# Kernel tuning notes

Measured on AMD Instinct MI355X. Metric: run time of the kernel, lower is better.

The kernel has to match this reference:

```python
import jax, jax.numpy as jnp
import numpy as np

K = 4            # n_factors
AGG_PARAM = 0.5
EPS = 1e-12      # F.normalize eps


def _normalize(v):
    # F.normalize along last axis: v / max(||v||, eps)
    return v / jnp.maximum(jnp.linalg.norm(v, axis=-1, keepdims=True), EPS)


def _aggregate(x, nbrs, max_iter):
    # x: [b, n, d], nbrs: [n, m] with values in [0, n] (n -> zero pad row)
    b, n, d = x.shape
    m = nbrs.shape[-1]
    dd = d // K
    xk = _normalize(x.reshape(b, n, K, dd))            # [b,n,k,dd]
    z_src = jnp.concatenate(
        [xk.reshape(b, n, d), jnp.zeros((b, 1, d), x.dtype)], axis=1)
    z = z_src[:, nbrs.reshape(-1)].reshape(b, n, m, K, dd)  # gather neighbors
    u = None
    for it in range(max_iter):
        if u is None:
            p = jnp.full((b, n, m, K), 1.0 / K, x.dtype)  # softmax of zeros
        else:
            logits = jnp.einsum('bnmkd,bnkd->bnmk', z, u)
            p = jax.nn.softmax(logits, axis=3)
        u = jnp.einsum('bnmkd,bnmk->bnkd', z, p) + xk
        if it < max_iter - 1:
            u = _normalize(u)
    return u.reshape(b, n, d)


def setup_inputs() -> dict:
    key = jax.random.key(0)
    k1, k2 = jax.random.split(key)
    T, b, n, d, m = 3, 1, 50000, 64, 16
    x_all = jax.random.normal(k1, (T, b, n, d), dtype=jnp.float32)
    neighbors_all = jax.random.randint(k2, (T, n, m), 0, n, dtype=jnp.int64)
    return {"x_all": x_all, "neighbors_all": neighbors_all, "max_iter": 3}


def reference(x_all, neighbors_all, max_iter):
    T = x_all.shape[0]
    embs = []
    for t in range(T):
        x_temp = _aggregate(x_all[t], neighbors_all[t], max_iter)
        if t > 0:
            w = jax.nn.sigmoid(
                jnp.arange(t, dtype=x_all.dtype)).reshape(t, 1, 1, 1)
            e = (jnp.sum(w * jnp.stack(embs), axis=0) / t * AGG_PARAM
                 + x_temp * (1.0 - AGG_PARAM))
        else:
            e = x_temp
        embs.append(e)
    return jnp.stack(embs)  # [T, b, n, d]
```

## Files before the change

### kernel.cpp

```cpp
#include <hip/hip_runtime.h>


constexpr int T  = 3;
constexpr int N  = 50000;
constexpr int D  = 64;
constexpr int M  = 16;
constexpr float EPS2 = 1e-24f;

template <int CTRL>
__device__ __forceinline__ float dpp_add(float v) {
    int rot = __builtin_amdgcn_mov_dpp(__float_as_int(v), CTRL, 0xF, 0xF, false);
    return v + __int_as_float(rot);
}
__device__ __forceinline__ float rowsum16(float v) {
    v = dpp_add<0x128>(v);
    v = dpp_add<0x124>(v);
    v = dpp_add<0x122>(v);
    v = dpp_add<0x121>(v);
    return v;
}

__global__ __launch_bounds__(256, 4) void eaconv_fused(
    const float* __restrict__ x_all,
    const int*   __restrict__ nbr_all,
    float*       __restrict__ out)
{
    __shared__ float zb[4][M * D];
    __shared__ float ub[4][D];
    __shared__ float wb[4][D];
    const int wv   = threadIdx.x >> 6;
    const int i    = blockIdx.x * 4 + wv;
    const int lane = threadIdx.x & 63;
    if (i >= N) return;
    const int p  = lane & 15;
    const int k  = lane >> 4;
    const int x7 = p & 7;
    float* zw = zb[wv];
    float* uw = ub[wv];
    float* wwp = wb[wv];

    const int gq = lane >> 2;
    const int ge = lane & 3;
    const int c4 = (4 * k) ^ x7;

    float acc = 0.f;
    const float s1q = 0.25f * 0.7310585786300049f;

#pragma unroll
    for (int t = 0; t < T; ++t) {
        const float* x = x_all + (size_t)t * N * D;
        int j = nbr_all[((size_t)t * N + i) * M + p];
        const bool valid = (unsigned)j < (unsigned)N;
        j = valid ? j : 0;

#pragma unroll
        for (int c = 0; c < 4; ++c) {
            const int mm = 4 * c + k;
            const int jr = __shfl(j, mm, 64);
            const float4 v = *(const float4*)(x + (size_t)jr * D + p * 4);
            *(float4*)&zw[mm * 64 + ((p ^ (mm & 7)) << 2)] = v;
        }

        const float xv = x[(size_t)i * D + lane];
        const float sx = rowsum16(xv * xv);
        const float xh = xv * __builtin_amdgcn_rsqf(fmaxf(sx, EPS2));

        float zrow[16];
#pragma unroll
        for (int q = 0; q < 4; ++q) {
            const float4 v = *(const float4*)&zw[p * 64 + ((c4 ^ q) << 2)];
            zrow[4*q+0] = v.x; zrow[4*q+1] = v.y;
            zrow[4*q+2] = v.z; zrow[4*q+3] = v.w;
        }
        float zr[16];
#pragma unroll
        for (int m = 0; m < 16; ++m)
            zr[m] = zw[m * 64 + ((gq ^ (m & 7)) << 2) + ge];

        float s0 = zrow[0]*zrow[0], s1 = zrow[1]*zrow[1],
              s2 = zrow[2]*zrow[2], s3 = zrow[3]*zrow[3];
#pragma unroll
        for (int q = 4; q < 16; q += 4) {
            s0 = fmaf(zrow[q+0], zrow[q+0], s0);
            s1 = fmaf(zrow[q+1], zrow[q+1], s1);
            s2 = fmaf(zrow[q+2], zrow[q+2], s2);
            s3 = fmaf(zrow[q+3], zrow[q+3], s3);
        }
        float rz = __builtin_amdgcn_rsqf(fmaxf((s0+s1)+(s2+s3), EPS2));
        if (!valid) rz = 0.f;

        wwp[k * 16 + p] = rz;
        float rzr[16];
#pragma unroll
        for (int q = 0; q < 4; ++q) {
            const float4 v = *(const float4*)&wwp[k * 16 + 4 * q];
            rzr[4*q+0] = v.x; rzr[4*q+1] = v.y;
            rzr[4*q+2] = v.z; rzr[4*q+3] = v.w;
        }
        float u = xh * 4.0f;
#pragma unroll
        for (int m = 0; m < 16; ++m) u = fmaf(rzr[m], zr[m], u);
        float inv = __builtin_amdgcn_rsqf(fmaxf(rowsum16(u * u), EPS2));
        uw[lane] = u;

#pragma unroll
        for (int it = 1; it < 3; ++it) {
            float urow[16];
#pragma unroll
            for (int q = 0; q < 4; ++q) {
                const float4 v = *(const float4*)&uw[k * 16 + 4 * q];
                urow[4*q+0] = v.x; urow[4*q+1] = v.y;
                urow[4*q+2] = v.z; urow[4*q+3] = v.w;
            }
            float d0 = zrow[0]*urow[0], d1 = zrow[1]*urow[1],
                  d2 = zrow[2]*urow[2], d3 = zrow[3]*urow[3];
#pragma unroll
            for (int q = 4; q < 16; q += 4) {
                d0 = fmaf(zrow[q+0], urow[q+0], d0);
                d1 = fmaf(zrow[q+1], urow[q+1], d1);
                d2 = fmaf(zrow[q+2], urow[q+2], d2);
                d3 = fmaf(zrow[q+3], urow[q+3], d3);
            }
            const float dot = (d0 + d1) + (d2 + d3);
            const float logit = dot * (rz * inv);
            const float e = __expf(logit);
            float es = e + __shfl_xor(e, 16, 64);
            es += __shfl_xor(es, 32, 64);
            const float wf = e * __builtin_amdgcn_rcpf(es) * rz;

            wwp[k * 16 + p] = wf;
            float wr[16];
#pragma unroll
            for (int q = 0; q < 4; ++q) {
                const float4 v = *(const float4*)&wwp[k * 16 + 4 * q];
                wr[4*q+0] = v.x; wr[4*q+1] = v.y;
                wr[4*q+2] = v.z; wr[4*q+3] = v.w;
            }
            u = xh;
#pragma unroll
            for (int m = 0; m < 16; ++m) u = fmaf(wr[m], zr[m], u);
            if (it < 2) {
                inv = __builtin_amdgcn_rsqf(fmaxf(rowsum16(u * u), EPS2));
                uw[lane] = u;
            }
        }

        float wout;
        if (t == 0)      { wout = u; acc = u; }
        else if (t == 1) { wout = 0.25f * acc + 0.5f * u;
                           acc = fmaf(s1q, wout, 0.125f * acc); }
        else             { wout = acc + 0.5f * u; }
        out[((size_t)t * N + i) * D + lane] = wout;
    }
}

extern "C" void kernel_launch(void* const* d_in, const int* in_sizes, int n_in,
                              void* d_out, int out_size, void* d_ws, size_t ws_size,
                              hipStream_t stream) {
    const float* x_all = (const float*)d_in[0];
    const int*   nbrs  = (const int*)d_in[1];
    float*       out   = (float*)d_out;

    const int blocks = (N + 3) / 4;
    eaconv_fused<<<blocks, 256, 0, stream>>>(x_all, nbrs, out);
}
```

Before: 183.4 us.

## Prefetch next timestep's neighbor gather and split LDS into two layouts

Loads the next timestep's neighbor indices, self row and neighbor rows into registers while the current timestep computes, so global gather latency overlaps with compute. Gathered rows are now written to two LDS buffers: a swizzled one for row reads and a padded (stride 65) one for column reads. This replaces the XOR-swizzled column access and is meant to cut bank conflicts and address math. It costs more LDS per block and more live registers (four float4 prefetch buffers), which may reduce occupancy.

```diff
diff --git a/kernel.cpp b/kernel.cpp
--- a/kernel.cpp
+++ b/kernel.cpp
@@ -25,7 +25,8 @@
     const int*   __restrict__ nbr_all,
     float*       __restrict__ out)
 {
-    __shared__ float zb[4][M * D];
+    __shared__ float zs[4][M * 64];
+    __shared__ float zp[4][M * 65];
     __shared__ float ub[4][D];
     __shared__ float wb[4][D];
     const int wv   = threadIdx.x >> 6;
@@ -35,47 +36,76 @@
     const int p  = lane & 15;
     const int k  = lane >> 4;
     const int x7 = p & 7;
-    float* zw = zb[wv];
-    float* uw = ub[wv];
+    char* zsb = (char*)zs[wv];
+    char* zpb = (char*)zp[wv];
+    float* uw  = ub[wv];
     float* wwp = wb[wv];
 
-    const int gq = lane >> 2;
-    const int ge = lane & 3;
-    const int c4 = (4 * k) ^ x7;
+    const int ve  = 256 * k + 16 * (p ^ k);
+    const int vo  = ve ^ 64;
+    const int vpw = 260 * k + 16 * p;
+    const int c4  = (4 * k) ^ x7;
+    const int rq0 = 256 * p + ((c4 ^ 0) << 4);
+    const int rq1 = 256 * p + ((c4 ^ 1) << 4);
+    const int rq2 = 256 * p + ((c4 ^ 2) << 4);
+    const int rq3 = 256 * p + ((c4 ^ 3) << 4);
+    const int colb = 4 * lane;
+    const int rowb = 64 * k;
 
     float acc = 0.f;
     const float s1q = 0.25f * 0.7310585786300049f;
 
+    int jc; bool valid; float xv; float4 g0, g1, g2, g3;
+    {
+        const int jr = nbr_all[(size_t)i * M + p];
+        valid = (unsigned)jr < (unsigned)N;
+        jc = valid ? jr : 0;
+        xv = x_all[(size_t)i * D + lane];
+        const int j0 = __shfl(jc,      k, 64), j1 = __shfl(jc,  4 + k, 64),
+                  j2 = __shfl(jc,  8 + k, 64), j3 = __shfl(jc, 12 + k, 64);
+        g0 = *(const float4*)(x_all + (size_t)j0 * D + 4 * p);
+        g1 = *(const float4*)(x_all + (size_t)j1 * D + 4 * p);
+        g2 = *(const float4*)(x_all + (size_t)j2 * D + 4 * p);
+        g3 = *(const float4*)(x_all + (size_t)j3 * D + 4 * p);
+    }
+
 #pragma unroll
     for (int t = 0; t < T; ++t) {
-        const float* x = x_all + (size_t)t * N * D;
-        int j = nbr_all[((size_t)t * N + i) * M + p];
-        const bool valid = (unsigned)j < (unsigned)N;
-        j = valid ? j : 0;
-
-#pragma unroll
-        for (int c = 0; c < 4; ++c) {
-            const int mm = 4 * c + k;
-            const int jr = __shfl(j, mm, 64);
-            const float4 v = *(const float4*)(x + (size_t)jr * D + p * 4);
-            *(float4*)&zw[mm * 64 + ((p ^ (mm & 7)) << 2)] = v;
-        }
-
-        const float xv = x[(size_t)i * D + lane];
+        *(float4*)(zsb + ve)         = g0;
+        *(float4*)(zsb + vo + 1024)  = g1;
+        *(float4*)(zsb + ve + 2048)  = g2;
+        *(float4*)(zsb + vo + 3072)  = g3;
+        *(float4*)(zpb + vpw)        = g0;
+        *(float4*)(zpb + vpw + 1040) = g1;
+        *(float4*)(zpb + vpw + 2080) = g2;
+        *(float4*)(zpb + vpw + 3120) = g3;
+
+        int jn = 0; bool nvalid = false; float xn = 0.f;
+        if (t < T - 1) {
+            const int jr = nbr_all[((size_t)(t + 1) * N + i) * M + p];
+            nvalid = (unsigned)jr < (unsigned)N;
+            jn = nvalid ? jr : 0;
+            xn = x_all[((size_t)(t + 1) * N + i) * D + lane];
+        }
+
         const float sx = rowsum16(xv * xv);
         const float xh = xv * __builtin_amdgcn_rsqf(fmaxf(sx, EPS2));
 
         float zrow[16];
-#pragma unroll
-        for (int q = 0; q < 4; ++q) {
-            const float4 v = *(const float4*)&zw[p * 64 + ((c4 ^ q) << 2)];
-            zrow[4*q+0] = v.x; zrow[4*q+1] = v.y;
-            zrow[4*q+2] = v.z; zrow[4*q+3] = v.w;
+        {
+            const float4 v0 = *(const float4*)(zsb + rq0);
+            const float4 v1 = *(const float4*)(zsb + rq1);
+            const float4 v2 = *(const float4*)(zsb + rq2);
+            const float4 v3 = *(const float4*)(zsb + rq3);
+            zrow[ 0]=v0.x; zrow[ 1]=v0.y; zrow[ 2]=v0.z; zrow[ 3]=v0.w;
+            zrow[ 4]=v1.x; zrow[ 5]=v1.y; zrow[ 6]=v1.z; zrow[ 7]=v1.w;
+            zrow[ 8]=v2.x; zrow[ 9]=v2.y; zrow[10]=v2.z; zrow[11]=v2.w;
+            zrow[12]=v3.x; zrow[13]=v3.y; zrow[14]=v3.z; zrow[15]=v3.w;
         }
         float zr[16];
 #pragma unroll
         for (int m = 0; m < 16; ++m)
-            zr[m] = zw[m * 64 + ((gq ^ (m & 7)) << 2) + ge];
+            zr[m] = *(const float*)(zpb + colb + 260 * m);
 
         float s0 = zrow[0]*zrow[0], s1 = zrow[1]*zrow[1],
               s2 = zrow[2]*zrow[2], s3 = zrow[3]*zrow[3];
@@ -89,13 +119,17 @@
         float rz = __builtin_amdgcn_rsqf(fmaxf((s0+s1)+(s2+s3), EPS2));
         if (!valid) rz = 0.f;
 
-        wwp[k * 16 + p] = rz;
+        wwp[lane] = rz;
         float rzr[16];
-#pragma unroll
-        for (int q = 0; q < 4; ++q) {
-            const float4 v = *(const float4*)&wwp[k * 16 + 4 * q];
-            rzr[4*q+0] = v.x; rzr[4*q+1] = v.y;
-            rzr[4*q+2] = v.z; rzr[4*q+3] = v.w;
+        {
+            const float4 v0 = *(const float4*)((char*)wwp + rowb);
+            const float4 v1 = *(const float4*)((char*)wwp + rowb + 16);
+            const float4 v2 = *(const float4*)((char*)wwp + rowb + 32);
+            const float4 v3 = *(const float4*)((char*)wwp + rowb + 48);
+            rzr[ 0]=v0.x; rzr[ 1]=v0.y; rzr[ 2]=v0.z; rzr[ 3]=v0.w;
+            rzr[ 4]=v1.x; rzr[ 5]=v1.y; rzr[ 6]=v1.z; rzr[ 7]=v1.w;
+            rzr[ 8]=v2.x; rzr[ 9]=v2.y; rzr[10]=v2.z; rzr[11]=v2.w;
+            rzr[12]=v3.x; rzr[13]=v3.y; rzr[14]=v3.z; rzr[15]=v3.w;
         }
         float u = xh * 4.0f;
 #pragma unroll
@@ -103,14 +137,28 @@
         float inv = __builtin_amdgcn_rsqf(fmaxf(rowsum16(u * u), EPS2));
         uw[lane] = u;
 
+        if (t < T - 1) {
+            const float* xnp = x_all + (size_t)(t + 1) * N * D;
+            const int j0 = __shfl(jn,      k, 64), j1 = __shfl(jn,  4 + k, 64),
+                      j2 = __shfl(jn,  8 + k, 64), j3 = __shfl(jn, 12 + k, 64);
+            g0 = *(const float4*)(xnp + (size_t)j0 * D + 4 * p);
+            g1 = *(const float4*)(xnp + (size_t)j1 * D + 4 * p);
+            g2 = *(const float4*)(xnp + (size_t)j2 * D + 4 * p);
+            g3 = *(const float4*)(xnp + (size_t)j3 * D + 4 * p);
+        }
+
 #pragma unroll
         for (int it = 1; it < 3; ++it) {
             float urow[16];
-#pragma unroll
-            for (int q = 0; q < 4; ++q) {
-                const float4 v = *(const float4*)&uw[k * 16 + 4 * q];
-                urow[4*q+0] = v.x; urow[4*q+1] = v.y;
-                urow[4*q+2] = v.z; urow[4*q+3] = v.w;
+            {
+                const float4 v0 = *(const float4*)((char*)uw + rowb);
+                const float4 v1 = *(const float4*)((char*)uw + rowb + 16);
+                const float4 v2 = *(const float4*)((char*)uw + rowb + 32);
+                const float4 v3 = *(const float4*)((char*)uw + rowb + 48);
+                urow[ 0]=v0.x; urow[ 1]=v0.y; urow[ 2]=v0.z; urow[ 3]=v0.w;
+                urow[ 4]=v1.x; urow[ 5]=v1.y; urow[ 6]=v1.z; urow[ 7]=v1.w;
+                urow[ 8]=v2.x; urow[ 9]=v2.y; urow[10]=v2.z; urow[11]=v2.w;
+                urow[12]=v3.x; urow[13]=v3.y; urow[14]=v3.z; urow[15]=v3.w;
             }
             float d0 = zrow[0]*urow[0], d1 = zrow[1]*urow[1],
                   d2 = zrow[2]*urow[2], d3 = zrow[3]*urow[3];
@@ -128,13 +176,17 @@
             es += __shfl_xor(es, 32, 64);
             const float wf = e * __builtin_amdgcn_rcpf(es) * rz;
 
-            wwp[k * 16 + p] = wf;
+            wwp[lane] = wf;
             float wr[16];
-#pragma unroll
-            for (int q = 0; q < 4; ++q) {
-                const float4 v = *(const float4*)&wwp[k * 16 + 4 * q];
-                wr[4*q+0] = v.x; wr[4*q+1] = v.y;
-                wr[4*q+2] = v.z; wr[4*q+3] = v.w;
+            {
+                const float4 v0 = *(const float4*)((char*)wwp + rowb);
+                const float4 v1 = *(const float4*)((char*)wwp + rowb + 16);
+                const float4 v2 = *(const float4*)((char*)wwp + rowb + 32);
+                const float4 v3 = *(const float4*)((char*)wwp + rowb + 48);
+                wr[ 0]=v0.x; wr[ 1]=v0.y; wr[ 2]=v0.z; wr[ 3]=v0.w;
+                wr[ 4]=v1.x; wr[ 5]=v1.y; wr[ 6]=v1.z; wr[ 7]=v1.w;
+                wr[ 8]=v2.x; wr[ 9]=v2.y; wr[10]=v2.z; wr[11]=v2.w;
+                wr[12]=v3.x; wr[13]=v3.y; wr[14]=v3.z; wr[15]=v3.w;
             }
             u = xh;
 #pragma unroll
@@ -151,6 +203,8 @@
                            acc = fmaf(s1q, wout, 0.125f * acc); }
         else             { wout = acc + 0.5f * u; }
         out[((size_t)t * N + i) * D + lane] = wout;
+
+        jc = jn; valid = nvalid; xv = xn;
     }
 }
 
```

Result: slower. 200.4 us (+9.3%).

## Keep per-neighbor factor rows in registers and reduce via DPP instead of LDS

Applied to the files above, without the earlier changes.

Each lane now loads its own neighbor row's four float4 chunks directly, reading them in a strided order. It also keeps a full 16-element factor row of x, z and u in registers. Cross-neighbor sums use rowsum16 DPP reductions instead of LDS round-trips for the rz, softmax weight and u arrays, which removes two shared buffers and several LDS writes and reads per iteration. The cost is more DPP reduction ops per element (16 rowsums per iteration), higher register pressure, and output stores from only 4 lanes per row. The bounds check is dropped, which relies on N being divisible by 4.

```diff
diff --git a/kernel.cpp b/kernel.cpp
--- a/kernel.cpp
+++ b/kernel.cpp
@@ -1,10 +1,10 @@
 #include <hip/hip_runtime.h>
 
 
-constexpr int T  = 3;
-constexpr int N  = 50000;
-constexpr int D  = 64;
-constexpr int M  = 16;
+constexpr int T = 3;
+constexpr int N = 50000;
+constexpr int D = 64;
+constexpr int M = 16;
 constexpr float EPS2 = 1e-24f;
 
 template <int CTRL>
@@ -25,25 +25,26 @@
     const int*   __restrict__ nbr_all,
     float*       __restrict__ out)
 {
-    __shared__ float zb[4][M * D];
-    __shared__ float ub[4][D];
-    __shared__ float wb[4][D];
+    __shared__ float zs[4][M * 64];
     const int wv   = threadIdx.x >> 6;
     const int i    = blockIdx.x * 4 + wv;
     const int lane = threadIdx.x & 63;
-    if (i >= N) return;
     const int p  = lane & 15;
     const int k  = lane >> 4;
     const int x7 = p & 7;
-    float* zw = zb[wv];
-    float* uw = ub[wv];
-    float* wwp = wb[wv];
+    char* zsb = (char*)zs[wv];
 
-    const int gq = lane >> 2;
-    const int ge = lane & 3;
-    const int c4 = (4 * k) ^ x7;
+    const int wa0 = 256 * p + (((k     ) ^ x7) << 4);
+    const int wa1 = 256 * p + (((k |  4) ^ x7) << 4);
+    const int wa2 = 256 * p + (((k |  8) ^ x7) << 4);
+    const int wa3 = 256 * p + (((k | 12) ^ x7) << 4);
+    const int c4  = (4 * k) ^ x7;
+    const int ra0 = 256 * p + ((c4 ^ 0) << 4);
+    const int ra1 = 256 * p + ((c4 ^ 1) << 4);
+    const int ra2 = 256 * p + ((c4 ^ 2) << 4);
+    const int ra3 = 256 * p + ((c4 ^ 3) << 4);
 
-    float acc = 0.f;
+    float accr[16];
     const float s1q = 0.25f * 0.7310585786300049f;
 
 #pragma unroll
@@ -53,104 +54,122 @@
         const bool valid = (unsigned)j < (unsigned)N;
         j = valid ? j : 0;
 
-#pragma unroll
-        for (int c = 0; c < 4; ++c) {
-            const int mm = 4 * c + k;
-            const int jr = __shfl(j, mm, 64);
-            const float4 v = *(const float4*)(x + (size_t)jr * D + p * 4);
-            *(float4*)&zw[mm * 64 + ((p ^ (mm & 7)) << 2)] = v;
-        }
+        const float* zbase = x + (size_t)j * D + 4 * k;
+        const float4 g0 = *(const float4*)(zbase +  0);
+        const float4 g1 = *(const float4*)(zbase + 16);
+        const float4 g2 = *(const float4*)(zbase + 32);
+        const float4 g3 = *(const float4*)(zbase + 48);
 
-        const float xv = x[(size_t)i * D + lane];
-        const float sx = rowsum16(xv * xv);
-        const float xh = xv * __builtin_amdgcn_rsqf(fmaxf(sx, EPS2));
+        const float4* xr4 = (const float4*)(x + (size_t)i * D + 16 * k);
+        const float4 h0 = xr4[0], h1 = xr4[1], h2 = xr4[2], h3 = xr4[3];
 
-        float zrow[16];
-#pragma unroll
-        for (int q = 0; q < 4; ++q) {
-            const float4 v = *(const float4*)&zw[p * 64 + ((c4 ^ q) << 2)];
-            zrow[4*q+0] = v.x; zrow[4*q+1] = v.y;
-            zrow[4*q+2] = v.z; zrow[4*q+3] = v.w;
-        }
-        float zr[16];
-#pragma unroll
-        for (int m = 0; m < 16; ++m)
-            zr[m] = zw[m * 64 + ((gq ^ (m & 7)) << 2) + ge];
+        *(float4*)(zsb + wa0) = g0;
+        *(float4*)(zsb + wa1) = g1;
+        *(float4*)(zsb + wa2) = g2;
+        *(float4*)(zsb + wa3) = g3;
 
-        float s0 = zrow[0]*zrow[0], s1 = zrow[1]*zrow[1],
-              s2 = zrow[2]*zrow[2], s3 = zrow[3]*zrow[3];
+        float xh[16] = {h0.x,h0.y,h0.z,h0.w, h1.x,h1.y,h1.z,h1.w,
+                        h2.x,h2.y,h2.z,h2.w, h3.x,h3.y,h3.z,h3.w};
+        float a0 = xh[0]*xh[0], a1 = xh[1]*xh[1],
+              a2 = xh[2]*xh[2], a3 = xh[3]*xh[3];
 #pragma unroll
         for (int q = 4; q < 16; q += 4) {
-            s0 = fmaf(zrow[q+0], zrow[q+0], s0);
-            s1 = fmaf(zrow[q+1], zrow[q+1], s1);
-            s2 = fmaf(zrow[q+2], zrow[q+2], s2);
-            s3 = fmaf(zrow[q+3], zrow[q+3], s3);
+            a0 = fmaf(xh[q+0], xh[q+0], a0);
+            a1 = fmaf(xh[q+1], xh[q+1], a1);
+            a2 = fmaf(xh[q+2], xh[q+2], a2);
+            a3 = fmaf(xh[q+3], xh[q+3], a3);
         }
-        float rz = __builtin_amdgcn_rsqf(fmaxf((s0+s1)+(s2+s3), EPS2));
+        const float rx = __builtin_amdgcn_rsqf(fmaxf((a0+a1)+(a2+a3), EPS2));
+#pragma unroll
+        for (int q = 0; q < 16; ++q) xh[q] *= rx;
+
+        const float4 z0 = *(const float4*)(zsb + ra0);
+        const float4 z1 = *(const float4*)(zsb + ra1);
+        const float4 z2 = *(const float4*)(zsb + ra2);
+        const float4 z3 = *(const float4*)(zsb + ra3);
+        float zh[16] = {z0.x,z0.y,z0.z,z0.w, z1.x,z1.y,z1.z,z1.w,
+                        z2.x,z2.y,z2.z,z2.w, z3.x,z3.y,z3.z,z3.w};
+        float b0 = zh[0]*zh[0], b1 = zh[1]*zh[1],
+              b2 = zh[2]*zh[2], b3 = zh[3]*zh[3];
+#pragma unroll
+        for (int q = 4; q < 16; q += 4) {
+            b0 = fmaf(zh[q+0], zh[q+0], b0);
+            b1 = fmaf(zh[q+1], zh[q+1], b1);
+            b2 = fmaf(zh[q+2], zh[q+2], b2);
+            b3 = fmaf(zh[q+3], zh[q+3], b3);
+        }
+        float rz = __builtin_amdgcn_rsqf(fmaxf((b0+b1)+(b2+b3), EPS2));
         if (!valid) rz = 0.f;
+#pragma unroll
+        for (int q = 0; q < 16; ++q) zh[q] *= rz;
 
-        wwp[k * 16 + p] = rz;
-        float rzr[16];
+        float ur[16];
 #pragma unroll
-        for (int q = 0; q < 4; ++q) {
-            const float4 v = *(const float4*)&wwp[k * 16 + 4 * q];
-            rzr[4*q+0] = v.x; rzr[4*q+1] = v.y;
-            rzr[4*q+2] = v.z; rzr[4*q+3] = v.w;
+        for (int q = 0; q < 16; ++q)
+            ur[q] = fmaf(xh[q], 4.0f, rowsum16(zh[q]));
+        float n0 = ur[0]*ur[0], n1 = ur[1]*ur[1],
+              n2 = ur[2]*ur[2], n3 = ur[3]*ur[3];
+#pragma unroll
+        for (int q = 4; q < 16; q += 4) {
+            n0 = fmaf(ur[q+0], ur[q+0], n0);
+            n1 = fmaf(ur[q+1], ur[q+1], n1);
+            n2 = fmaf(ur[q+2], ur[q+2], n2);
+            n3 = fmaf(ur[q+3], ur[q+3], n3);
         }
-        float u = xh * 4.0f;
-#pragma unroll
-        for (int m = 0; m < 16; ++m) u = fmaf(rzr[m], zr[m], u);
-        float inv = __builtin_amdgcn_rsqf(fmaxf(rowsum16(u * u), EPS2));
-        uw[lane] = u;
+        float inv = __builtin_amdgcn_rsqf(fmaxf((n0+n1)+(n2+n3), EPS2));
 
 #pragma unroll
         for (int it = 1; it < 3; ++it) {
-            float urow[16];
-#pragma unroll
-            for (int q = 0; q < 4; ++q) {
-                const float4 v = *(const float4*)&uw[k * 16 + 4 * q];
-                urow[4*q+0] = v.x; urow[4*q+1] = v.y;
-                urow[4*q+2] = v.z; urow[4*q+3] = v.w;
-            }
-            float d0 = zrow[0]*urow[0], d1 = zrow[1]*urow[1],
-                  d2 = zrow[2]*urow[2], d3 = zrow[3]*urow[3];
+            float d0 = zh[0]*ur[0], d1 = zh[1]*ur[1],
+                  d2 = zh[2]*ur[2], d3 = zh[3]*ur[3];
 #pragma unroll
             for (int q = 4; q < 16; q += 4) {
-                d0 = fmaf(zrow[q+0], urow[q+0], d0);
-                d1 = fmaf(zrow[q+1], urow[q+1], d1);
-                d2 = fmaf(zrow[q+2], urow[q+2], d2);
-                d3 = fmaf(zrow[q+3], urow[q+3], d3);
+                d0 = fmaf(zh[q+0], ur[q+0], d0);
+                d1 = fmaf(zh[q+1], ur[q+1], d1);
+                d2 = fmaf(zh[q+2], ur[q+2], d2);
+                d3 = fmaf(zh[q+3], ur[q+3], d3);
             }
-            const float dot = (d0 + d1) + (d2 + d3);
-            const float logit = dot * (rz * inv);
+            const float logit = ((d0+d1)+(d2+d3)) * inv;
             const float e = __expf(logit);
             float es = e + __shfl_xor(e, 16, 64);
             es += __shfl_xor(es, 32, 64);
-            const float wf = e * __builtin_amdgcn_rcpf(es) * rz;
-
-            wwp[k * 16 + p] = wf;
-            float wr[16];
+            const float wf = e * __builtin_amdgcn_rcpf(es);
 #pragma unroll
-            for (int q = 0; q < 4; ++q) {
-                const float4 v = *(const float4*)&wwp[k * 16 + 4 * q];
-                wr[4*q+0] = v.x; wr[4*q+1] = v.y;
-                wr[4*q+2] = v.z; wr[4*q+3] = v.w;
-            }
-            u = xh;
+            for (int q = 0; q < 16; ++q)
+                ur[q] = xh[q] + rowsum16(zh[q] * wf);
+            if (it < 2) {
+                float m0 = ur[0]*ur[0], m1 = ur[1]*ur[1],
+                      m2 = ur[2]*ur[2], m3 = ur[3]*ur[3];
 #pragma unroll
-            for (int m = 0; m < 16; ++m) u = fmaf(wr[m], zr[m], u);
-            if (it < 2) {
-                inv = __builtin_amdgcn_rsqf(fmaxf(rowsum16(u * u), EPS2));
-                uw[lane] = u;
+                for (int q = 4; q < 16; q += 4) {
+                    m0 = fmaf(ur[q+0], ur[q+0], m0);
+                    m1 = fmaf(ur[q+1], ur[q+1], m1);
+                    m2 = fmaf(ur[q+2], ur[q+2], m2);
+                    m3 = fmaf(ur[q+3], ur[q+3], m3);
+                }
+                inv = __builtin_amdgcn_rsqf(fmaxf((m0+m1)+(m2+m3), EPS2));
             }
         }
 
-        float wout;
-        if (t == 0)      { wout = u; acc = u; }
-        else if (t == 1) { wout = 0.25f * acc + 0.5f * u;
-                           acc = fmaf(s1q, wout, 0.125f * acc); }
-        else             { wout = acc + 0.5f * u; }
-        out[((size_t)t * N + i) * D + lane] = wout;
+        float wout[16];
+        if (t == 0) {
+#pragma unroll
+            for (int q = 0; q < 16; ++q) { wout[q] = ur[q]; accr[q] = ur[q]; }
+        } else if (t == 1) {
+#pragma unroll
+            for (int q = 0; q < 16; ++q) {
+                wout[q] = 0.25f * accr[q] + 0.5f * ur[q];
+                accr[q] = fmaf(s1q, wout[q], 0.125f * accr[q]);
+            }
+        } else {
+#pragma unroll
+            for (int q = 0; q < 16; ++q) wout[q] = accr[q] + 0.5f * ur[q];
+        }
+        float* o = out + ((size_t)t * N + i) * D + 16 * k;
+        if (p == 0) ((float4*)o)[0] = make_float4(wout[0],  wout[1],  wout[2],  wout[3]);
+        if (p == 1) ((float4*)o)[1] = make_float4(wout[4],  wout[5],  wout[6],  wout[7]);
+        if (p == 2) ((float4*)o)[2] = make_float4(wout[8],  wout[9],  wout[10], wout[11]);
+        if (p == 3) ((float4*)o)[3] = make_float4(wout[12], wout[13], wout[14], wout[15]);
     }
 }
 
@@ -161,6 +180,5 @@
     const int*   nbrs  = (const int*)d_in[1];
     float*       out   = (float*)d_out;
 
-    const int blocks = (N + 3) / 4;
-    eaconv_fused<<<blocks, 256, 0, stream>>>(x_all, nbrs, out);
+    eaconv_fused<<<N / 4, 256, 0, stream>>>(x_all, nbrs, out);
 }
```

New measurement: 236.6 us. +29.0%, slower.

## Gather neighbor rows straight from global memory instead of staging through LDS

Applied to the files above, without the earlier changes.

Drops the 16 KB shared-memory staging buffer for the gathered neighbor rows. Each lane now loads its column of every neighbor row from global memory using wave-uniform row indices from readlane, and loads its own neighbor's factor slice a second time with float4 reads. Neighbor vectors are pre-scaled by their inverse norms, so the rz multiplies in the routing iterations go away. The N bounds check is also removed. This cuts LDS traffic and frees LDS for more resident waves, at the cost of reading neighbor rows twice through the cache.

```diff
diff --git a/kernel.cpp b/kernel.cpp
--- a/kernel.cpp
+++ b/kernel.cpp
@@ -1,10 +1,10 @@
 #include <hip/hip_runtime.h>
 
 
-constexpr int T  = 3;
-constexpr int N  = 50000;
-constexpr int D  = 64;
-constexpr int M  = 16;
+constexpr int T = 3;
+constexpr int N = 50000;
+constexpr int D = 64;
+constexpr int M = 16;
 constexpr float EPS2 = 1e-24f;
 
 template <int CTRL>
@@ -25,23 +25,16 @@
     const int*   __restrict__ nbr_all,
     float*       __restrict__ out)
 {
-    __shared__ float zb[4][M * D];
     __shared__ float ub[4][D];
     __shared__ float wb[4][D];
     const int wv   = threadIdx.x >> 6;
     const int i    = blockIdx.x * 4 + wv;
     const int lane = threadIdx.x & 63;
-    if (i >= N) return;
     const int p  = lane & 15;
     const int k  = lane >> 4;
-    const int x7 = p & 7;
-    float* zw = zb[wv];
-    float* uw = ub[wv];
+    float* uw  = ub[wv];
     float* wwp = wb[wv];
-
-    const int gq = lane >> 2;
-    const int ge = lane & 3;
-    const int c4 = (4 * k) ^ x7;
+    const int rowb = 64 * k;
 
     float acc = 0.f;
     const float s1q = 0.25f * 0.7310585786300049f;
@@ -53,64 +46,74 @@
         const bool valid = (unsigned)j < (unsigned)N;
         j = valid ? j : 0;
 
+        float zr[16];
 #pragma unroll
-        for (int c = 0; c < 4; ++c) {
-            const int mm = 4 * c + k;
-            const int jr = __shfl(j, mm, 64);
-            const float4 v = *(const float4*)(x + (size_t)jr * D + p * 4);
-            *(float4*)&zw[mm * 64 + ((p ^ (mm & 7)) << 2)] = v;
+        for (int m = 0; m < 16; ++m) {
+            const int jm = __builtin_amdgcn_readlane(j, m);
+            zr[m] = x[(size_t)jm * D + lane];
         }
+
+        const float* zrp = x + (size_t)j * D + 16 * k;
+        const float4 r0 = *(const float4*)(zrp + 0);
+        const float4 r1 = *(const float4*)(zrp + 4);
+        const float4 r2 = *(const float4*)(zrp + 8);
+        const float4 r3 = *(const float4*)(zrp + 12);
+        float zrow[16] = {r0.x,r0.y,r0.z,r0.w, r1.x,r1.y,r1.z,r1.w,
+                          r2.x,r2.y,r2.z,r2.w, r3.x,r3.y,r3.z,r3.w};
 
         const float xv = x[(size_t)i * D + lane];
         const float sx = rowsum16(xv * xv);
         const float xh = xv * __builtin_amdgcn_rsqf(fmaxf(sx, EPS2));
 
-        float zrow[16];
-#pragma unroll
-        for (int q = 0; q < 4; ++q) {
-            const float4 v = *(const float4*)&zw[p * 64 + ((c4 ^ q) << 2)];
-            zrow[4*q+0] = v.x; zrow[4*q+1] = v.y;
-            zrow[4*q+2] = v.z; zrow[4*q+3] = v.w;
-        }
-        float zr[16];
-#pragma unroll
-        for (int m = 0; m < 16; ++m)
-            zr[m] = zw[m * 64 + ((gq ^ (m & 7)) << 2) + ge];
-
-        float s0 = zrow[0]*zrow[0], s1 = zrow[1]*zrow[1],
-              s2 = zrow[2]*zrow[2], s3 = zrow[3]*zrow[3];
+        float b0 = zrow[0]*zrow[0], b1 = zrow[1]*zrow[1],
+              b2 = zrow[2]*zrow[2], b3 = zrow[3]*zrow[3];
 #pragma unroll
         for (int q = 4; q < 16; q += 4) {
-            s0 = fmaf(zrow[q+0], zrow[q+0], s0);
-            s1 = fmaf(zrow[q+1], zrow[q+1], s1);
-            s2 = fmaf(zrow[q+2], zrow[q+2], s2);
-            s3 = fmaf(zrow[q+3], zrow[q+3], s3);
+            b0 = fmaf(zrow[q+0], zrow[q+0], b0);
+            b1 = fmaf(zrow[q+1], zrow[q+1], b1);
+            b2 = fmaf(zrow[q+2], zrow[q+2], b2);
+            b3 = fmaf(zrow[q+3], zrow[q+3], b3);
         }
-        float rz = __builtin_amdgcn_rsqf(fmaxf((s0+s1)+(s2+s3), EPS2));
+        float rz = __builtin_amdgcn_rsqf(fmaxf((b0+b1)+(b2+b3), EPS2));
         if (!valid) rz = 0.f;
+#pragma unroll
+        for (int q = 0; q < 16; ++q) zrow[q] *= rz;
 
-        wwp[k * 16 + p] = rz;
+        wwp[lane] = rz;
         float rzr[16];
+        {
+            const float4 v0 = *(const float4*)((char*)wwp + rowb);
+            const float4 v1 = *(const float4*)((char*)wwp + rowb + 16);
+            const float4 v2 = *(const float4*)((char*)wwp + rowb + 32);
+            const float4 v3 = *(const float4*)((char*)wwp + rowb + 48);
+            rzr[ 0]=v0.x; rzr[ 1]=v0.y; rzr[ 2]=v0.z; rzr[ 3]=v0.w;
+            rzr[ 4]=v1.x; rzr[ 5]=v1.y; rzr[ 6]=v1.z; rzr[ 7]=v1.w;
+            rzr[ 8]=v2.x; rzr[ 9]=v2.y; rzr[10]=v2.z; rzr[11]=v2.w;
+            rzr[12]=v3.x; rzr[13]=v3.y; rzr[14]=v3.z; rzr[15]=v3.w;
+        }
 #pragma unroll
-        for (int q = 0; q < 4; ++q) {
-            const float4 v = *(const float4*)&wwp[k * 16 + 4 * q];
-            rzr[4*q+0] = v.x; rzr[4*q+1] = v.y;
-            rzr[4*q+2] = v.z; rzr[4*q+3] = v.w;
-        }
-        float u = xh * 4.0f;
-#pragma unroll
-        for (int m = 0; m < 16; ++m) u = fmaf(rzr[m], zr[m], u);
+        for (int m = 0; m < 16; ++m) zr[m] *= rzr[m];
+
+        float t0a = zr[0]+zr[1], t0b = zr[2]+zr[3], t0c = zr[4]+zr[5],
+              t0d = zr[6]+zr[7], t0e = zr[8]+zr[9], t0f = zr[10]+zr[11],
+              t0g = zr[12]+zr[13], t0h = zr[14]+zr[15];
+        float u = fmaf(xh, 4.0f,
+                       ((t0a+t0b)+(t0c+t0d)) + ((t0e+t0f)+(t0g+t0h)));
         float inv = __builtin_amdgcn_rsqf(fmaxf(rowsum16(u * u), EPS2));
         uw[lane] = u;
 
 #pragma unroll
         for (int it = 1; it < 3; ++it) {
             float urow[16];
-#pragma unroll
-            for (int q = 0; q < 4; ++q) {
-                const float4 v = *(const float4*)&uw[k * 16 + 4 * q];
-                urow[4*q+0] = v.x; urow[4*q+1] = v.y;
-                urow[4*q+2] = v.z; urow[4*q+3] = v.w;
+            {
+                const float4 v0 = *(const float4*)((char*)uw + rowb);
+                const float4 v1 = *(const float4*)((char*)uw + rowb + 16);
+                const float4 v2 = *(const float4*)((char*)uw + rowb + 32);
+                const float4 v3 = *(const float4*)((char*)uw + rowb + 48);
+                urow[ 0]=v0.x; urow[ 1]=v0.y; urow[ 2]=v0.z; urow[ 3]=v0.w;
+                urow[ 4]=v1.x; urow[ 5]=v1.y; urow[ 6]=v1.z; urow[ 7]=v1.w;
+                urow[ 8]=v2.x; urow[ 9]=v2.y; urow[10]=v2.z; urow[11]=v2.w;
+                urow[12]=v3.x; urow[13]=v3.y; urow[14]=v3.z; urow[15]=v3.w;
             }
             float d0 = zrow[0]*urow[0], d1 = zrow[1]*urow[1],
                   d2 = zrow[2]*urow[2], d3 = zrow[3]*urow[3];
@@ -121,24 +124,27 @@
                 d2 = fmaf(zrow[q+2], urow[q+2], d2);
                 d3 = fmaf(zrow[q+3], urow[q+3], d3);
             }
-            const float dot = (d0 + d1) + (d2 + d3);
-            const float logit = dot * (rz * inv);
+            const float logit = ((d0+d1)+(d2+d3)) * inv;
             const float e = __expf(logit);
             float es = e + __shfl_xor(e, 16, 64);
             es += __shfl_xor(es, 32, 64);
-            const float wf = e * __builtin_amdgcn_rcpf(es) * rz;
+            const float wf = e * __builtin_amdgcn_rcpf(es);
 
-            wwp[k * 16 + p] = wf;
-            float wr[16];
-#pragma unroll
-            for (int q = 0; q < 4; ++q) {
-                const float4 v = *(const float4*)&wwp[k * 16 + 4 * q];
-                wr[4*q+0] = v.x; wr[4*q+1] = v.y;
-                wr[4*q+2] = v.z; wr[4*q+3] = v.w;
+            wwp[lane] = wf;
+            float wfr[16];
+            {
+                const float4 v0 = *(const float4*)((char*)wwp + rowb);
+                const float4 v1 = *(const float4*)((char*)wwp + rowb + 16);
+                const float4 v2 = *(const float4*)((char*)wwp + rowb + 32);
+                const float4 v3 = *(const float4*)((char*)wwp + rowb + 48);
+                wfr[ 0]=v0.x; wfr[ 1]=v0.y; wfr[ 2]=v0.z; wfr[ 3]=v0.w;
+                wfr[ 4]=v1.x; wfr[ 5]=v1.y; wfr[ 6]=v1.z; wfr[ 7]=v1.w;
+                wfr[ 8]=v2.x; wfr[ 9]=v2.y; wfr[10]=v2.z; wfr[11]=v2.w;
+                wfr[12]=v3.x; wfr[13]=v3.y; wfr[14]=v3.z; wfr[15]=v3.w;
             }
             u = xh;
 #pragma unroll
-            for (int m = 0; m < 16; ++m) u = fmaf(wr[m], zr[m], u);
+            for (int m = 0; m < 16; ++m) u = fmaf(wfr[m], zr[m], u);
             if (it < 2) {
                 inv = __builtin_amdgcn_rsqf(fmaxf(rowsum16(u * u), EPS2));
                 uw[lane] = u;
@@ -161,6 +167,5 @@
     const int*   nbrs  = (const int*)d_in[1];
     float*       out   = (float*)d_out;
 
-    const int blocks = (N + 3) / 4;
-    eaconv_fused<<<blocks, 256, 0, stream>>>(x_all, nbrs, out);
+    eaconv_fused<<<N / 4, 256, 0, stream>>>(x_all, nbrs, out);
 }
```

Result: slower. 188.8 us (+3.0%).
